# Kernel optimization log

Hardware: AMD Instinct MI355X
Metric: run time of the kernel (lower is better)

Reference implementation:

```python
import jax, jax.numpy as jnp
import numpy as np

MAX_ITER = 3


def setup_inputs() -> dict:
    key = jax.random.key(0)
    k1, k2, k3, k4 = jax.random.split(key, 4)
    B, S = 2, 160
    return {
        "s_edge": jax.random.normal(k1, (B, S, S), dtype=jnp.float32),
        "s_sib": jax.random.normal(k2, (B, S, S, S), dtype=jnp.float32),
        "s_cop": jax.random.normal(k3, (B, S, S, S), dtype=jnp.float32),
        "s_grd": jax.random.normal(k4, (B, S, S, S), dtype=jnp.float32),
        "mask": jnp.ones((B, S, S), dtype=bool),
    }


def _belief_propagation(s_edge, s_sib, s_cop, s_grd, mask):
    B, S, _ = mask.shape
    idx = jnp.arange(S)
    i, j = idx[:, None], idx[None, :]
    hs = jnp.minimum(i, j)  # [S,S] = min(index_i, index_j)
    ms = jnp.maximum(i, j)  # [S,S]

    mask_t = jnp.transpose(mask, (2, 1, 0))  # [S,S,B]
    # mask2o[x,y,z,b] = mask_t[x,z,b] & mask_t[x,y,b] & (hs[x,y]!=z) & (ms[x,y]!=z)
    mask2o = mask_t[:, None, :, :] & mask_t[:, :, None, :]
    mask2o = mask2o & (hs[:, :, None] != idx)[:, :, :, None]
    mask2o = mask2o & (ms[:, :, None] != idx)[:, :, :, None]
    mask2o_f = mask2o.astype(s_edge.dtype)  # [S,S,S,B]

    # p_edge[k,j,i,b] = (k==1) * s_edge[b,i,j]
    p_edge = jnp.transpose(jnp.stack([jnp.zeros_like(s_edge), s_edge]), (0, 3, 2, 1))  # [2,S,S,B]
    p_sib = jnp.transpose(s_sib, (2, 1, 3, 0))  # [S,S,S,B]
    p_cop = jnp.transpose(s_cop, (2, 1, 3, 0))
    p_grd = jnp.transpose(s_grd, (2, 1, 3, 0))

    b = jnp.zeros((2, S, S, B), dtype=s_edge.dtype)
    m_sib = jnp.zeros((2, S, S, S, B), dtype=s_edge.dtype)
    m_cop = jnp.zeros_like(m_sib)
    m_grd = jnp.zeros_like(m_sib)

    def update(b, m_prev, p):
        m = b[:, :, :, None, :] - m_prev  # [2,S,S,S,B]
        m0 = jnp.logaddexp(m[0], m[1])
        m1 = jnp.logaddexp(m[0], m[1] + p)
        mm = jnp.swapaxes(jnp.stack([m0, m1]), 2, 3)
        return jax.nn.log_softmax(mm, axis=0)

    for _ in range(MAX_ITER):
        b = jax.nn.log_softmax(b, axis=0)
        m_sib = update(b, m_sib, p_sib)
        m_cop = update(b, m_cop, p_cop)
        m_grd = update(b, m_grd, p_grd)
        b = p_edge + jnp.sum((m_sib + m_cop + m_grd) * mask2o_f, axis=3)

    # [B,S,S,2] log-marginals
    return jax.nn.log_softmax(jnp.transpose(b, (3, 2, 1, 0)), axis=-1)


def reference(s_edge, s_sib, s_cop, s_grd, mask):
    logQ = _belief_propagation(s_edge, s_sib, s_cop, s_grd, mask)
    return jnp.exp(logQ)  # marginals [B,S,S,2]
```

## Files before the change

kernel.cpp:

```cpp
#include <hip/hip_runtime.h>
#include <hip/hip_fp16.h>


#define S    160
#define S2   25600
#define S3   4096000
#define STR  162
#define C2E  1.4426950408889634f

__device__ __forceinline__ float fexp2(float x) { return __builtin_amdgcn_exp2f(x); }
__device__ __forceinline__ float flog2(float x) { return __builtin_amdgcn_logf(x); }
__device__ __forceinline__ float frcp(float x)  { return __builtin_amdgcn_rcpf(x); }
__device__ __forceinline__ float cdb(float x) {
    return fminf(fmaxf(x, -45.f), 45.f);
}
__device__ __forceinline__ float sp2t(float tp) { return flog2(1.f + tp); }
__device__ __forceinline__ float Ff(float x, float tp) {
    float tx = fexp2(x);
    return flog2(1.f + tx * tp) - flog2(1.f + tx);
}
__device__ __forceinline__ const float* selT(int t, const float* a,
                                             const float* b, const float* c) {
    return (t == 0) ? a : (t == 1) ? b : c;
}

__global__ __launch_bounds__(960)
void k_fused(const float* __restrict__ s_sib, const float* __restrict__ s_cop,
             const float* __restrict__ s_grd, const float* __restrict__ s_edge,
             float* __restrict__ outp)
{
    int slice = blockIdx.x;
    int a = slice % S, n = slice / S;
    int tid = threadIdx.x;
    int u4 = tid % 40, r = tid / 40;
    int us = tid % S,  vs = tid / S;

    __shared__ __half tp3[3 * S * STR];
    __shared__ float  scr[1280];
    __shared__ float  db1s[S], db2s[S], E1[S], E2[S];

    float4 acc = make_float4(0.f, 0.f, 0.f, 0.f);
    float edg = 0.f;
    if (tid < S) edg = s_edge[n * S2 + tid * S + a] * C2E;
    #pragma unroll
    for (int t = 0; t < 3; ++t) {
        const float* g = selT(t, s_sib, s_cop, s_grd)
                       + (long)n * S3 + (long)a * S + u4 * 4;
        float4 pv[7];
        #pragma unroll
        for (int i = 0; i < 6; ++i)
            pv[i] = *(const float4*)(g + (long)(r + 24 * i) * S2);
        if (r < 16) pv[6] = *(const float4*)(g + (long)(r + 144) * S2);
        float4 P = make_float4(1.f, 1.f, 1.f, 1.f);
        #pragma unroll
        for (int i = 0; i < 7; ++i) {
            if (i == 6 && r >= 16) break;
            int v = r + 24 * i;
            float t0 = fexp2(pv[i].x * C2E), t1 = fexp2(pv[i].y * C2E);
            float t2 = fexp2(pv[i].z * C2E), t3 = fexp2(pv[i].w * C2E);
            P.x = __builtin_fmaf(P.x, t0, P.x);
            P.y = __builtin_fmaf(P.y, t1, P.y);
            P.z = __builtin_fmaf(P.z, t2, P.z);
            P.w = __builtin_fmaf(P.w, t3, P.w);
            __half* b = &tp3[t * (S * STR) + v * STR + u4 * 4];
            *(__half2*)(b)     = __floats2half2_rn(t0, t1);
            *(__half2*)(b + 2) = __floats2half2_rn(t2, t3);
        }
        acc.x += flog2(P.x); acc.y += flog2(P.y);
        acc.z += flog2(P.z); acc.w += flog2(P.w);
    }
    float4* scr4 = (float4*)scr;
    if (r < 8) scr4[r * 40 + u4] = acc;
    __syncthreads();
    if (r >= 8 && r < 16) {
        float4 o = scr4[(r - 8) * 40 + u4];
        o.x += acc.x; o.y += acc.y; o.z += acc.z; o.w += acc.w;
        scr4[(r - 8) * 40 + u4] = o;
    }
    __syncthreads();
    if (r >= 16) {
        float4 o = scr4[(r - 16) * 40 + u4];
        o.x += acc.x; o.y += acc.y; o.z += acc.z; o.w += acc.w;
        scr4[(r - 16) * 40 + u4] = o;
    }
    __syncthreads();
    if (tid < S) {
        int u = tid, cu4 = u >> 2, cc = u & 3;
        float s = 0.f;
        #pragma unroll
        for (int g2 = 0; g2 < 8; ++g2) s += scr[(g2 * 40 + cu4) * 4 + cc];
        float rr = edg + s - 480.f;
        #pragma unroll
        for (int t = 0; t < 3; ++t) {
            const __half* sl = &tp3[t * (S * STR)];
            float tpa = __half2float(sl[a * STR + u]);
            rr -= (sp2t(tpa) - 1.f);
            if (u != a) {
                float tpu = __half2float(sl[u * STR + u]);
                rr -= (sp2t(tpu) - 1.f);
            }
        }
        db1s[u] = rr;
        E1[u] = fexp2(cdb(rr) + 1.f);
    }
    __syncthreads();

    float d2acc = 0.f;
    #pragma unroll
    for (int t = 0; t < 3; ++t) {
        const __half* sl = &tp3[t * (S * STR)];
        for (int kb = 0; kb < 6; ++kb) {
            float tA[4], tB[4], Ev[4];
            #pragma unroll
            for (int j = 0; j < 4; ++j) {
                int v = (kb * 4 + j) * 6 + vs;
                tA[j] = __half2float(sl[v * STR + us]);
                tB[j] = __half2float(sl[us * STR + v]);
                Ev[j] = E1[v];
            }
            #pragma unroll
            for (int j = 0; j < 4; ++j) {
                float B1 = 1.f + tB[j];
                float nm = __builtin_fmaf(Ev[j], tA[j], B1);
                float dn = B1 + Ev[j];
                d2acc += flog2(nm) - flog2(dn);
            }
        }
        #pragma unroll
        for (int k = 24; k < 27; ++k) {
            int v = k * 6 + vs;
            if (v < S) {
                float tA = __half2float(sl[v * STR + us]);
                float tB = __half2float(sl[us * STR + v]);
                float B1 = 1.f + tB;
                float nm = __builtin_fmaf(E1[v], tA, B1);
                float dn = B1 + E1[v];
                d2acc += flog2(nm) - flog2(dn);
            }
        }
    }
    scr[vs * S + us] = d2acc;
    __syncthreads();
    if (tid < S) {
        int u = tid;
        float sw = scr[u] + scr[S + u] + scr[2 * S + u] + scr[3 * S + u]
                 + scr[4 * S + u] + scr[5 * S + u];
        float db1a1 = cdb(db1s[a]) + 1.f;
        float db1u1 = cdb(db1s[u]) + 1.f;
        float sum = 0.f;
        #pragma unroll
        for (int t = 0; t < 3; ++t) {
            const __half* sl = &tp3[t * (S * STR)];
            float tpa  = __half2float(sl[a * STR + u]);
            float tpba = __half2float(sl[u * STR + a]);
            sum += Ff(db1a1 - sp2t(tpba), tpa);
            if (u != a) {
                float tpu = __half2float(sl[u * STR + u]);
                sum += Ff(db1u1 - sp2t(tpu), tpu);
            }
        }
        float d2v = edg - sum + sw;
        db2s[u] = d2v;
        E2[u] = fexp2(cdb(d2v));
    }
    __syncthreads();

    float d3acc = 0.f;
    float E1u = E1[us];
    #pragma unroll
    for (int t = 0; t < 3; ++t) {
        const __half* sl = &tp3[t * (S * STR)];
        for (int kb = 0; kb < 6; ++kb) {
            float tA[4], tB[4], Ev[4];
            #pragma unroll
            for (int j = 0; j < 4; ++j) {
                int v = (kb * 4 + j) * 6 + vs;
                tA[j] = __half2float(sl[v * STR + us]);
                tB[j] = __half2float(sl[us * STR + v]);
                Ev[j] = E2[v];
            }
            #pragma unroll
            for (int j = 0; j < 4; ++j) {
                float A1 = 1.f + tA[j];
                float q  = A1 + E1u;
                float rr = __builtin_fmaf(E1u, tB[j], A1);
                float p  = Ev[j] * q;
                float nm = __builtin_fmaf(p, tA[j], rr);
                float dn = rr + p;
                d3acc += flog2(nm) - flog2(dn);
            }
        }
        #pragma unroll
        for (int k = 24; k < 27; ++k) {
            int v = k * 6 + vs;
            if (v < S) {
                float tA = __half2float(sl[v * STR + us]);
                float tB = __half2float(sl[us * STR + v]);
                float A1 = 1.f + tA;
                float q  = A1 + E1u;
                float rr = __builtin_fmaf(E1u, tB, A1);
                float p  = E2[v] * q;
                float nm = __builtin_fmaf(p, tA, rr);
                float dn = rr + p;
                d3acc += flog2(nm) - flog2(dn);
            }
        }
    }
    scr[vs * S + us] = d3acc;
    __syncthreads();
    if (tid < S) {
        int u = tid;
        float sw = scr[u] + scr[S + u] + scr[2 * S + u] + scr[3 * S + u]
                 + scr[4 * S + u] + scr[5 * S + u];
        float db1u1 = cdb(db1s[u]) + 1.f;
        float db2a = cdb(db2s[a]);
        float db2u = cdb(db2s[u]);
        float sum = 0.f;
        #pragma unroll
        for (int t = 0; t < 3; ++t) {
            const __half* sl = &tp3[t * (S * STR)];
            float tpa  = __half2float(sl[a * STR + u]);
            float tpba = __half2float(sl[u * STR + a]);
            float d2vu = Ff(db1u1 - sp2t(tpa), tpba);
            sum += Ff(db2a - d2vu, tpa);
            if (u != a) {
                float tpu = __half2float(sl[u * STR + u]);
                float d2  = Ff(db1u1 - sp2t(tpu), tpu);
                sum += Ff(db2u - d2, tpu);
            }
        }
        float s = edg - sum + sw;
        float sc  = fminf(fmaxf(s, -60.f), 60.f);
        float tsg = fexp2(-sc);
        float rr  = __fdividef(1.f, 1.f + tsg);
        long ob = ((long)(n * S + u) * S + a) * 2;
        *(float2*)(outp + ob) = make_float2(tsg * rr, rr);
    }
}

extern "C" void kernel_launch(void* const* d_in, const int* in_sizes, int n_in,
                              void* d_out, int out_size, void* d_ws, size_t ws_size,
                              hipStream_t stream) {
    const float* s_edge = (const float*)d_in[0];
    const float* s_sib  = (const float*)d_in[1];
    const float* s_cop  = (const float*)d_in[2];
    const float* s_grd  = (const float*)d_in[3];
    float* outp = (float*)d_out;
    (void)d_ws; (void)ws_size;

    k_fused<<<320, 960, 0, stream>>>(s_sib, s_cop, s_grd, s_edge, outp);
}
```

Before: 155.5 us.

## Process both batch slices per block, prefetching second batch into registers

Each block now handles both batch elements for one column index a, halving the grid to 160 blocks. The second batch's score loads and exp2 work are issued up front and held as packed half values in registers, then written to shared memory after the first batch finishes. This overlaps the second load with the first batch's compute. The d2 inner loop also pairs log2 calls by multiplying two arguments before one log. The risks are lower occupancy on a 256-CU device, since only 160 blocks run, plus heavy register pressure from 21 uint2 per thread.

Result: no change. 156.9 us (+0.9%).

```diff
diff --git a/kernel.cpp b/kernel.cpp
--- a/kernel.cpp
+++ b/kernel.cpp
@@ -10,7 +10,6 @@
 
 __device__ __forceinline__ float fexp2(float x) { return __builtin_amdgcn_exp2f(x); }
 __device__ __forceinline__ float flog2(float x) { return __builtin_amdgcn_logf(x); }
-__device__ __forceinline__ float frcp(float x)  { return __builtin_amdgcn_rcpf(x); }
 __device__ __forceinline__ float cdb(float x) {
     return fminf(fmaxf(x, -45.f), 45.f);
 }
@@ -29,8 +28,7 @@
              const float* __restrict__ s_grd, const float* __restrict__ s_edge,
              float* __restrict__ outp)
 {
-    int slice = blockIdx.x;
-    int a = slice % S, n = slice / S;
+    int a = blockIdx.x;
     int tid = threadIdx.x;
     int u4 = tid % 40, r = tid / 40;
     int us = tid % S,  vs = tid / S;
@@ -39,13 +37,10 @@
     __shared__ float  scr[1280];
     __shared__ float  db1s[S], db2s[S], E1[S], E2[S];
 
-    float4 acc = make_float4(0.f, 0.f, 0.f, 0.f);
-    float edg = 0.f;
-    if (tid < S) edg = s_edge[n * S2 + tid * S + a] * C2E;
+    float4 acc0 = make_float4(0.f, 0.f, 0.f, 0.f);
     #pragma unroll
     for (int t = 0; t < 3; ++t) {
-        const float* g = selT(t, s_sib, s_cop, s_grd)
-                       + (long)n * S3 + (long)a * S + u4 * 4;
+        const float* g = selT(t, s_sib, s_cop, s_grd) + (long)a * S + u4 * 4;
         float4 pv[7];
         #pragma unroll
         for (int i = 0; i < 6; ++i)
@@ -66,175 +61,227 @@
             *(__half2*)(b)     = __floats2half2_rn(t0, t1);
             *(__half2*)(b + 2) = __floats2half2_rn(t2, t3);
         }
-        acc.x += flog2(P.x); acc.y += flog2(P.y);
-        acc.z += flog2(P.z); acc.w += flog2(P.w);
-    }
-    float4* scr4 = (float4*)scr;
-    if (r < 8) scr4[r * 40 + u4] = acc;
-    __syncthreads();
-    if (r >= 8 && r < 16) {
-        float4 o = scr4[(r - 8) * 40 + u4];
-        o.x += acc.x; o.y += acc.y; o.z += acc.z; o.w += acc.w;
-        scr4[(r - 8) * 40 + u4] = o;
-    }
-    __syncthreads();
-    if (r >= 16) {
-        float4 o = scr4[(r - 16) * 40 + u4];
-        o.x += acc.x; o.y += acc.y; o.z += acc.z; o.w += acc.w;
-        scr4[(r - 16) * 40 + u4] = o;
-    }
-    __syncthreads();
+        acc0.x += flog2(P.x); acc0.y += flog2(P.y);
+        acc0.z += flog2(P.z); acc0.w += flog2(P.w);
+    }
+    float4 acc1 = make_float4(0.f, 0.f, 0.f, 0.f);
+    uint2 ha1[21];
+    #pragma unroll
+    for (int t = 0; t < 3; ++t) {
+        const float* g = selT(t, s_sib, s_cop, s_grd) + S3 + (long)a * S + u4 * 4;
+        float4 pv[7];
+        #pragma unroll
+        for (int i = 0; i < 6; ++i)
+            pv[i] = *(const float4*)(g + (long)(r + 24 * i) * S2);
+        if (r < 16) pv[6] = *(const float4*)(g + (long)(r + 144) * S2);
+        float4 P = make_float4(1.f, 1.f, 1.f, 1.f);
+        #pragma unroll
+        for (int i = 0; i < 7; ++i) {
+            if (i == 6 && r >= 16) break;
+            float t0 = fexp2(pv[i].x * C2E), t1 = fexp2(pv[i].y * C2E);
+            float t2 = fexp2(pv[i].z * C2E), t3 = fexp2(pv[i].w * C2E);
+            P.x = __builtin_fmaf(P.x, t0, P.x);
+            P.y = __builtin_fmaf(P.y, t1, P.y);
+            P.z = __builtin_fmaf(P.z, t2, P.z);
+            P.w = __builtin_fmaf(P.w, t3, P.w);
+            __half2 h01 = __floats2half2_rn(t0, t1);
+            __half2 h23 = __floats2half2_rn(t2, t3);
+            ha1[t * 7 + i].x = *(unsigned*)&h01;
+            ha1[t * 7 + i].y = *(unsigned*)&h23;
+        }
+        acc1.x += flog2(P.x); acc1.y += flog2(P.y);
+        acc1.z += flog2(P.z); acc1.w += flog2(P.w);
+    }
+    float edg0 = 0.f, edg1 = 0.f;
     if (tid < S) {
-        int u = tid, cu4 = u >> 2, cc = u & 3;
-        float s = 0.f;
-        #pragma unroll
-        for (int g2 = 0; g2 < 8; ++g2) s += scr[(g2 * 40 + cu4) * 4 + cc];
-        float rr = edg + s - 480.f;
+        edg0 = s_edge[tid * S + a] * C2E;
+        edg1 = s_edge[S2 + tid * S + a] * C2E;
+    }
+
+    #pragma unroll 1
+    for (int ns = 0; ns < 2; ++ns) {
+        if (ns == 1) {
+            #pragma unroll
+            for (int t = 0; t < 3; ++t)
+                #pragma unroll
+                for (int i = 0; i < 7; ++i) {
+                    if (i == 6 && r >= 16) break;
+                    int v = r + 24 * i;
+                    *(uint2*)(&tp3[t * (S * STR) + v * STR + u4 * 4]) = ha1[t * 7 + i];
+                }
+            __syncthreads();
+        }
+        float4 accC = ns ? acc1 : acc0;
+        float  edgC = ns ? edg1 : edg0;
+        float4* scr4 = (float4*)scr;
+        if (r < 8) scr4[r * 40 + u4] = accC;
+        __syncthreads();
+        if (r >= 8 && r < 16) {
+            float4 o = scr4[(r - 8) * 40 + u4];
+            o.x += accC.x; o.y += accC.y; o.z += accC.z; o.w += accC.w;
+            scr4[(r - 8) * 40 + u4] = o;
+        }
+        __syncthreads();
+        if (r >= 16) {
+            float4 o = scr4[(r - 16) * 40 + u4];
+            o.x += accC.x; o.y += accC.y; o.z += accC.z; o.w += accC.w;
+            scr4[(r - 16) * 40 + u4] = o;
+        }
+        __syncthreads();
+        if (tid < S) {
+            int u = tid, cu4 = u >> 2, cc = u & 3;
+            float s = 0.f;
+            #pragma unroll
+            for (int g2 = 0; g2 < 8; ++g2) s += scr[(g2 * 40 + cu4) * 4 + cc];
+            float rr = edgC + s - 480.f;
+            #pragma unroll
+            for (int t = 0; t < 3; ++t) {
+                const __half* sl = &tp3[t * (S * STR)];
+                float tpa = __half2float(sl[a * STR + u]);
+                rr -= (sp2t(tpa) - 1.f);
+                if (u != a) {
+                    float tpu = __half2float(sl[u * STR + u]);
+                    rr -= (sp2t(tpu) - 1.f);
+                }
+            }
+            db1s[u] = rr;
+            E1[u] = fexp2(cdb(rr) + 1.f);
+        }
+        __syncthreads();
+
+        float d2acc = 0.f;
         #pragma unroll
         for (int t = 0; t < 3; ++t) {
             const __half* sl = &tp3[t * (S * STR)];
-            float tpa = __half2float(sl[a * STR + u]);
-            rr -= (sp2t(tpa) - 1.f);
-            if (u != a) {
-                float tpu = __half2float(sl[u * STR + u]);
-                rr -= (sp2t(tpu) - 1.f);
-            }
-        }
-        db1s[u] = rr;
-        E1[u] = fexp2(cdb(rr) + 1.f);
-    }
-    __syncthreads();
-
-    float d2acc = 0.f;
-    #pragma unroll
-    for (int t = 0; t < 3; ++t) {
-        const __half* sl = &tp3[t * (S * STR)];
-        for (int kb = 0; kb < 6; ++kb) {
-            float tA[4], tB[4], Ev[4];
-            #pragma unroll
-            for (int j = 0; j < 4; ++j) {
-                int v = (kb * 4 + j) * 6 + vs;
-                tA[j] = __half2float(sl[v * STR + us]);
-                tB[j] = __half2float(sl[us * STR + v]);
-                Ev[j] = E1[v];
-            }
-            #pragma unroll
-            for (int j = 0; j < 4; ++j) {
-                float B1 = 1.f + tB[j];
-                float nm = __builtin_fmaf(Ev[j], tA[j], B1);
-                float dn = B1 + Ev[j];
-                d2acc += flog2(nm) - flog2(dn);
-            }
-        }
-        #pragma unroll
-        for (int k = 24; k < 27; ++k) {
-            int v = k * 6 + vs;
-            if (v < S) {
-                float tA = __half2float(sl[v * STR + us]);
-                float tB = __half2float(sl[us * STR + v]);
-                float B1 = 1.f + tB;
-                float nm = __builtin_fmaf(E1[v], tA, B1);
-                float dn = B1 + E1[v];
-                d2acc += flog2(nm) - flog2(dn);
-            }
-        }
-    }
-    scr[vs * S + us] = d2acc;
-    __syncthreads();
-    if (tid < S) {
-        int u = tid;
-        float sw = scr[u] + scr[S + u] + scr[2 * S + u] + scr[3 * S + u]
-                 + scr[4 * S + u] + scr[5 * S + u];
-        float db1a1 = cdb(db1s[a]) + 1.f;
-        float db1u1 = cdb(db1s[u]) + 1.f;
-        float sum = 0.f;
+            for (int kb = 0; kb < 6; ++kb) {
+                float tA[4], tB[4], Ev[4], nm[4], dn[4];
+                #pragma unroll
+                for (int j = 0; j < 4; ++j) {
+                    int v = (kb * 4 + j) * 6 + vs;
+                    tA[j] = __half2float(sl[v * STR + us]);
+                    tB[j] = __half2float(sl[us * STR + v]);
+                    Ev[j] = E1[v];
+                }
+                #pragma unroll
+                for (int j = 0; j < 4; ++j) {
+                    float B1 = 1.f + tB[j];
+                    nm[j] = __builtin_fmaf(Ev[j], tA[j], B1);
+                    dn[j] = B1 + Ev[j];
+                }
+                d2acc += flog2(nm[0] * nm[1]) - flog2(dn[0] * dn[1]);
+                d2acc += flog2(nm[2] * nm[3]) - flog2(dn[2] * dn[3]);
+            }
+            #pragma unroll
+            for (int k = 24; k < 27; ++k) {
+                int v = k * 6 + vs;
+                if (v < S) {
+                    float tA = __half2float(sl[v * STR + us]);
+                    float tB = __half2float(sl[us * STR + v]);
+                    float B1 = 1.f + tB;
+                    float nm = __builtin_fmaf(E1[v], tA, B1);
+                    float dn = B1 + E1[v];
+                    d2acc += flog2(nm) - flog2(dn);
+                }
+            }
+        }
+        scr[vs * S + us] = d2acc;
+        __syncthreads();
+        if (tid < S) {
+            int u = tid;
+            float sw = scr[u] + scr[S + u] + scr[2 * S + u] + scr[3 * S + u]
+                     + scr[4 * S + u] + scr[5 * S + u];
+            float db1a1 = cdb(db1s[a]) + 1.f;
+            float db1u1 = cdb(db1s[u]) + 1.f;
+            float sum = 0.f;
+            #pragma unroll
+            for (int t = 0; t < 3; ++t) {
+                const __half* sl = &tp3[t * (S * STR)];
+                float tpa  = __half2float(sl[a * STR + u]);
+                float tpba = __half2float(sl[u * STR + a]);
+                sum += Ff(db1a1 - sp2t(tpba), tpa);
+                if (u != a) {
+                    float tpu = __half2float(sl[u * STR + u]);
+                    sum += Ff(db1u1 - sp2t(tpu), tpu);
+                }
+            }
+            float d2v = edgC - sum + sw;
+            db2s[u] = d2v;
+            E2[u] = fexp2(cdb(d2v));
+        }
+        __syncthreads();
+
+        float d3acc = 0.f;
+        float E1u = E1[us];
         #pragma unroll
         for (int t = 0; t < 3; ++t) {
             const __half* sl = &tp3[t * (S * STR)];
-            float tpa  = __half2float(sl[a * STR + u]);
-            float tpba = __half2float(sl[u * STR + a]);
-            sum += Ff(db1a1 - sp2t(tpba), tpa);
-            if (u != a) {
-                float tpu = __half2float(sl[u * STR + u]);
-                sum += Ff(db1u1 - sp2t(tpu), tpu);
-            }
-        }
-        float d2v = edg - sum + sw;
-        db2s[u] = d2v;
-        E2[u] = fexp2(cdb(d2v));
-    }
-    __syncthreads();
-
-    float d3acc = 0.f;
-    float E1u = E1[us];
-    #pragma unroll
-    for (int t = 0; t < 3; ++t) {
-        const __half* sl = &tp3[t * (S * STR)];
-        for (int kb = 0; kb < 6; ++kb) {
-            float tA[4], tB[4], Ev[4];
-            #pragma unroll
-            for (int j = 0; j < 4; ++j) {
-                int v = (kb * 4 + j) * 6 + vs;
-                tA[j] = __half2float(sl[v * STR + us]);
-                tB[j] = __half2float(sl[us * STR + v]);
-                Ev[j] = E2[v];
-            }
-            #pragma unroll
-            for (int j = 0; j < 4; ++j) {
-                float A1 = 1.f + tA[j];
-                float q  = A1 + E1u;
-                float rr = __builtin_fmaf(E1u, tB[j], A1);
-                float p  = Ev[j] * q;
-                float nm = __builtin_fmaf(p, tA[j], rr);
-                float dn = rr + p;
-                d3acc += flog2(nm) - flog2(dn);
-            }
-        }
-        #pragma unroll
-        for (int k = 24; k < 27; ++k) {
-            int v = k * 6 + vs;
-            if (v < S) {
-                float tA = __half2float(sl[v * STR + us]);
-                float tB = __half2float(sl[us * STR + v]);
-                float A1 = 1.f + tA;
-                float q  = A1 + E1u;
-                float rr = __builtin_fmaf(E1u, tB, A1);
-                float p  = E2[v] * q;
-                float nm = __builtin_fmaf(p, tA, rr);
-                float dn = rr + p;
-                d3acc += flog2(nm) - flog2(dn);
-            }
-        }
-    }
-    scr[vs * S + us] = d3acc;
-    __syncthreads();
-    if (tid < S) {
-        int u = tid;
-        float sw = scr[u] + scr[S + u] + scr[2 * S + u] + scr[3 * S + u]
-                 + scr[4 * S + u] + scr[5 * S + u];
-        float db1u1 = cdb(db1s[u]) + 1.f;
-        float db2a = cdb(db2s[a]);
-        float db2u = cdb(db2s[u]);
-        float sum = 0.f;
-        #pragma unroll
-        for (int t = 0; t < 3; ++t) {
-            const __half* sl = &tp3[t * (S * STR)];
-            float tpa  = __half2float(sl[a * STR + u]);
-            float tpba = __half2float(sl[u * STR + a]);
-            float d2vu = Ff(db1u1 - sp2t(tpa), tpba);
-            sum += Ff(db2a - d2vu, tpa);
-            if (u != a) {
-                float tpu = __half2float(sl[u * STR + u]);
-                float d2  = Ff(db1u1 - sp2t(tpu), tpu);
-                sum += Ff(db2u - d2, tpu);
-            }
-        }
-        float s = edg - sum + sw;
-        float sc  = fminf(fmaxf(s, -60.f), 60.f);
-        float tsg = fexp2(-sc);
-        float rr  = __fdividef(1.f, 1.f + tsg);
-        long ob = ((long)(n * S + u) * S + a) * 2;
-        *(float2*)(outp + ob) = make_float2(tsg * rr, rr);
+            for (int kb = 0; kb < 6; ++kb) {
+                float tA[4], tB[4], Ev[4];
+                #pragma unroll
+                for (int j = 0; j < 4; ++j) {
+                    int v = (kb * 4 + j) * 6 + vs;
+                    tA[j] = __half2float(sl[v * STR + us]);
+                    tB[j] = __half2float(sl[us * STR + v]);
+                    Ev[j] = E2[v];
+                }
+                #pragma unroll
+                for (int j = 0; j < 4; ++j) {
+                    float A1 = 1.f + tA[j];
+                    float q  = A1 + E1u;
+                    float rr = __builtin_fmaf(E1u, tB[j], A1);
+                    float p  = Ev[j] * q;
+                    float nm = __builtin_fmaf(p, tA[j], rr);
+                    float dn = rr + p;
+                    d3acc += flog2(nm) - flog2(dn);
+                }
+            }
+            #pragma unroll
+            for (int k = 24; k < 27; ++k) {
+                int v = k * 6 + vs;
+                if (v < S) {
+                    float tA = __half2float(sl[v * STR + us]);
+                    float tB = __half2float(sl[us * STR + v]);
+                    float A1 = 1.f + tA;
+                    float q  = A1 + E1u;
+                    float rr = __builtin_fmaf(E1u, tB, A1);
+                    float p  = E2[v] * q;
+                    float nm = __builtin_fmaf(p, tA, rr);
+                    float dn = rr + p;
+                    d3acc += flog2(nm) - flog2(dn);
+                }
+            }
+        }
+        scr[vs * S + us] = d3acc;
+        __syncthreads();
+        if (tid < S) {
+            int u = tid;
+            float sw = scr[u] + scr[S + u] + scr[2 * S + u] + scr[3 * S + u]
+                     + scr[4 * S + u] + scr[5 * S + u];
+            float db1u1 = cdb(db1s[u]) + 1.f;
+            float db2a = cdb(db2s[a]);
+            float db2u = cdb(db2s[u]);
+            float sum = 0.f;
+            #pragma unroll
+            for (int t = 0; t < 3; ++t) {
+                const __half* sl = &tp3[t * (S * STR)];
+                float tpa  = __half2float(sl[a * STR + u]);
+                float tpba = __half2float(sl[u * STR + a]);
+                float d2vu = Ff(db1u1 - sp2t(tpa), tpba);
+                sum += Ff(db2a - d2vu, tpa);
+                if (u != a) {
+                    float tpu = __half2float(sl[u * STR + u]);
+                    float d2  = Ff(db1u1 - sp2t(tpu), tpu);
+                    sum += Ff(db2u - d2, tpu);
+                }
+            }
+            float s = edgC - sum + sw;
+            float sc  = fminf(fmaxf(s, -60.f), 60.f);
+            float tsg = fexp2(-sc);
+            float rr  = __fdividef(1.f, 1.f + tsg);
+            long ob = ((long)(ns * S + u) * S + a) * 2;
+            *(float2*)(outp + ob) = make_float2(tsg * rr, rr);
+        }
+        if (ns == 0) __syncthreads();
     }
 }
 
@@ -248,5 +295,5 @@
     float* outp = (float*)d_out;
     (void)d_ws; (void)ws_size;
 
-    k_fused<<<320, 960, 0, stream>>>(s_sib, s_cop, s_grd, s_edge, outp);
-}
+    k_fused<<<160, 960, 0, stream>>>(s_sib, s_cop, s_grd, s_edge, outp);
+}
```

## Use single shared slab and re-stream score tensors per phase

Applied to the files above, without the earlier changes.

Replaces the three resident half-precision score slabs in shared memory with a single slab. Each of the three factor types is reloaded from global memory and re-exponentiated before its pass in phases 2 and 3. The row, column and diagonal entries needed by the per-u epilogues are kept in small side arrays. The block drops from 960 to 640 threads, and the phase-2 log pairs are merged by multiplying before taking the log. This cuts shared memory use (which could allow more blocks per CU) at the cost of extra global reads, extra exp work and extra barriers.

New measurement: 172.6 us. +11.0%, slower.

```diff
diff --git a/kernel.cpp b/kernel.cpp
--- a/kernel.cpp
+++ b/kernel.cpp
@@ -10,7 +10,6 @@
 
 __device__ __forceinline__ float fexp2(float x) { return __builtin_amdgcn_exp2f(x); }
 __device__ __forceinline__ float flog2(float x) { return __builtin_amdgcn_logf(x); }
-__device__ __forceinline__ float frcp(float x)  { return __builtin_amdgcn_rcpf(x); }
 __device__ __forceinline__ float cdb(float x) {
     return fminf(fmaxf(x, -45.f), 45.f);
 }
@@ -23,8 +22,11 @@
                                              const float* b, const float* c) {
     return (t == 0) ? a : (t == 1) ? b : c;
 }
-
-__global__ __launch_bounds__(960)
+__device__ __forceinline__ __half hsel(__half2 h01, __half2 h23, int c) {
+    return (c == 0) ? h01.x : (c == 1) ? h01.y : (c == 2) ? h23.x : h23.y;
+}
+
+__global__ __launch_bounds__(640)
 void k_fused(const float* __restrict__ s_sib, const float* __restrict__ s_cop,
              const float* __restrict__ s_grd, const float* __restrict__ s_edge,
              float* __restrict__ outp)
@@ -35,68 +37,82 @@
     int u4 = tid % 40, r = tid / 40;
     int us = tid % S,  vs = tid / S;
 
-    __shared__ __half tp3[3 * S * STR];
+    __shared__ __half slab[S * STR];
     __shared__ float  scr[1280];
     __shared__ float  db1s[S], db2s[S], E1[S], E2[S];
+    __shared__ __half rowA[3][S], colA[3][S], diagA[3][S];
+
+    const int aq = a >> 2, ac = a & 3;
 
     float4 acc = make_float4(0.f, 0.f, 0.f, 0.f);
-    float edg = 0.f;
-    if (tid < S) edg = s_edge[n * S2 + tid * S + a] * C2E;
     #pragma unroll
     for (int t = 0; t < 3; ++t) {
         const float* g = selT(t, s_sib, s_cop, s_grd)
                        + (long)n * S3 + (long)a * S + u4 * 4;
-        float4 pv[7];
-        #pragma unroll
-        for (int i = 0; i < 6; ++i)
-            pv[i] = *(const float4*)(g + (long)(r + 24 * i) * S2);
-        if (r < 16) pv[6] = *(const float4*)(g + (long)(r + 144) * S2);
+        float4 pv[10];
+        #pragma unroll
+        for (int i = 0; i < 10; ++i)
+            pv[i] = *(const float4*)(g + (long)(r + 16 * i) * S2);
         float4 P = make_float4(1.f, 1.f, 1.f, 1.f);
-        #pragma unroll
-        for (int i = 0; i < 7; ++i) {
-            if (i == 6 && r >= 16) break;
-            int v = r + 24 * i;
+        float4 Q = make_float4(1.f, 1.f, 1.f, 1.f);
+        #pragma unroll
+        for (int i = 0; i < 10; ++i) {
+            int v = r + 16 * i;
             float t0 = fexp2(pv[i].x * C2E), t1 = fexp2(pv[i].y * C2E);
             float t2 = fexp2(pv[i].z * C2E), t3 = fexp2(pv[i].w * C2E);
-            P.x = __builtin_fmaf(P.x, t0, P.x);
-            P.y = __builtin_fmaf(P.y, t1, P.y);
-            P.z = __builtin_fmaf(P.z, t2, P.z);
-            P.w = __builtin_fmaf(P.w, t3, P.w);
-            __half* b = &tp3[t * (S * STR) + v * STR + u4 * 4];
-            *(__half2*)(b)     = __floats2half2_rn(t0, t1);
-            *(__half2*)(b + 2) = __floats2half2_rn(t2, t3);
-        }
-        acc.x += flog2(P.x); acc.y += flog2(P.y);
-        acc.z += flog2(P.z); acc.w += flog2(P.w);
-    }
+            if (i < 5) {
+                P.x = __builtin_fmaf(P.x, t0, P.x);
+                P.y = __builtin_fmaf(P.y, t1, P.y);
+                P.z = __builtin_fmaf(P.z, t2, P.z);
+                P.w = __builtin_fmaf(P.w, t3, P.w);
+            } else {
+                Q.x = __builtin_fmaf(Q.x, t0, Q.x);
+                Q.y = __builtin_fmaf(Q.y, t1, Q.y);
+                Q.z = __builtin_fmaf(Q.z, t2, Q.z);
+                Q.w = __builtin_fmaf(Q.w, t3, Q.w);
+            }
+            __half2 h01 = __floats2half2_rn(t0, t1);
+            __half2 h23 = __floats2half2_rn(t2, t3);
+            if (t == 2) {
+                uint2 w; w.x = *(unsigned*)&h01; w.y = *(unsigned*)&h23;
+                *(uint2*)(&slab[v * STR + u4 * 4]) = w;
+            }
+            if (v == a) {
+                uint2 w; w.x = *(unsigned*)&h01; w.y = *(unsigned*)&h23;
+                *(uint2*)(&rowA[t][u4 * 4]) = w;
+            }
+            if (u4 == aq) colA[t][v] = hsel(h01, h23, ac);
+            if (u4 == (v >> 2)) diagA[t][v] = hsel(h01, h23, v & 3);
+        }
+        acc.x += flog2(P.x) + flog2(Q.x);
+        acc.y += flog2(P.y) + flog2(Q.y);
+        acc.z += flog2(P.z) + flog2(Q.z);
+        acc.w += flog2(P.w) + flog2(Q.w);
+    }
+    float edg = 0.f;
+    if (tid < S) edg = s_edge[(long)n * S2 + tid * S + a] * C2E;
+    __syncthreads();
     float4* scr4 = (float4*)scr;
     if (r < 8) scr4[r * 40 + u4] = acc;
     __syncthreads();
-    if (r >= 8 && r < 16) {
+    if (r >= 8) {
         float4 o = scr4[(r - 8) * 40 + u4];
         o.x += acc.x; o.y += acc.y; o.z += acc.z; o.w += acc.w;
         scr4[(r - 8) * 40 + u4] = o;
     }
     __syncthreads();
-    if (r >= 16) {
-        float4 o = scr4[(r - 16) * 40 + u4];
-        o.x += acc.x; o.y += acc.y; o.z += acc.z; o.w += acc.w;
-        scr4[(r - 16) * 40 + u4] = o;
-    }
-    __syncthreads();
     if (tid < S) {
-        int u = tid, cu4 = u >> 2, cc = u & 3;
+        int u = tid;
         float s = 0.f;
         #pragma unroll
-        for (int g2 = 0; g2 < 8; ++g2) s += scr[(g2 * 40 + cu4) * 4 + cc];
+        for (int g2 = 0; g2 < 8; ++g2) s += scr[(g2 * 40 + (u >> 2)) * 4 + (u & 3)];
         float rr = edg + s - 480.f;
         #pragma unroll
         for (int t = 0; t < 3; ++t) {
-            const __half* sl = &tp3[t * (S * STR)];
-            float tpa = __half2float(sl[a * STR + u]);
+            float tpa = __half2float(rowA[t][u]);
             rr -= (sp2t(tpa) - 1.f);
             if (u != a) {
-                float tpu = __half2float(sl[u * STR + u]);
+                float tpu = __half2float(diagA[t][u]);
                 rr -= (sp2t(tpu) - 1.f);
             }
         }
@@ -106,56 +122,62 @@
     __syncthreads();
 
     float d2acc = 0.f;
-    #pragma unroll
-    for (int t = 0; t < 3; ++t) {
-        const __half* sl = &tp3[t * (S * STR)];
-        for (int kb = 0; kb < 6; ++kb) {
-            float tA[4], tB[4], Ev[4];
-            #pragma unroll
-            for (int j = 0; j < 4; ++j) {
-                int v = (kb * 4 + j) * 6 + vs;
-                tA[j] = __half2float(sl[v * STR + us]);
-                tB[j] = __half2float(sl[us * STR + v]);
+    #pragma unroll 1
+    for (int tt = 0; tt < 3; ++tt) {
+        int t = (tt == 0) ? 2 : tt - 1;
+        if (tt != 0) {
+            __syncthreads();
+            const float* g = selT(t, s_sib, s_cop, s_grd)
+                           + (long)n * S3 + (long)a * S + u4 * 4;
+            float4 pv[10];
+            #pragma unroll
+            for (int i = 0; i < 10; ++i)
+                pv[i] = *(const float4*)(g + (long)(r + 16 * i) * S2);
+            #pragma unroll
+            for (int i = 0; i < 10; ++i) {
+                float t0 = fexp2(pv[i].x * C2E), t1 = fexp2(pv[i].y * C2E);
+                float t2 = fexp2(pv[i].z * C2E), t3 = fexp2(pv[i].w * C2E);
+                __half2 h01 = __floats2half2_rn(t0, t1);
+                __half2 h23 = __floats2half2_rn(t2, t3);
+                uint2 w; w.x = *(unsigned*)&h01; w.y = *(unsigned*)&h23;
+                *(uint2*)(&slab[(r + 16 * i) * STR + u4 * 4]) = w;
+            }
+            __syncthreads();
+        }
+        for (int kb = 0; kb < 10; ++kb) {
+            float tA[4], tB[4], Ev[4], nm[4], dn[4];
+            #pragma unroll
+            for (int j = 0; j < 4; ++j) {
+                int v = kb * 16 + j * 4 + vs;
+                tA[j] = __half2float(slab[v * STR + us]);
+                tB[j] = __half2float(slab[us * STR + v]);
                 Ev[j] = E1[v];
             }
             #pragma unroll
             for (int j = 0; j < 4; ++j) {
                 float B1 = 1.f + tB[j];
-                float nm = __builtin_fmaf(Ev[j], tA[j], B1);
-                float dn = B1 + Ev[j];
-                d2acc += flog2(nm) - flog2(dn);
-            }
-        }
-        #pragma unroll
-        for (int k = 24; k < 27; ++k) {
-            int v = k * 6 + vs;
-            if (v < S) {
-                float tA = __half2float(sl[v * STR + us]);
-                float tB = __half2float(sl[us * STR + v]);
-                float B1 = 1.f + tB;
-                float nm = __builtin_fmaf(E1[v], tA, B1);
-                float dn = B1 + E1[v];
-                d2acc += flog2(nm) - flog2(dn);
-            }
+                nm[j] = __builtin_fmaf(Ev[j], tA[j], B1);
+                dn[j] = B1 + Ev[j];
+            }
+            d2acc += flog2(nm[0] * nm[1]) - flog2(dn[0] * dn[1]);
+            d2acc += flog2(nm[2] * nm[3]) - flog2(dn[2] * dn[3]);
         }
     }
     scr[vs * S + us] = d2acc;
     __syncthreads();
     if (tid < S) {
         int u = tid;
-        float sw = scr[u] + scr[S + u] + scr[2 * S + u] + scr[3 * S + u]
-                 + scr[4 * S + u] + scr[5 * S + u];
+        float sw = scr[u] + scr[S + u] + scr[2 * S + u] + scr[3 * S + u];
         float db1a1 = cdb(db1s[a]) + 1.f;
         float db1u1 = cdb(db1s[u]) + 1.f;
         float sum = 0.f;
         #pragma unroll
         for (int t = 0; t < 3; ++t) {
-            const __half* sl = &tp3[t * (S * STR)];
-            float tpa  = __half2float(sl[a * STR + u]);
-            float tpba = __half2float(sl[u * STR + a]);
+            float tpa  = __half2float(rowA[t][u]);
+            float tpba = __half2float(colA[t][u]);
             sum += Ff(db1a1 - sp2t(tpba), tpa);
             if (u != a) {
-                float tpu = __half2float(sl[u * STR + u]);
+                float tpu = __half2float(diagA[t][u]);
                 sum += Ff(db1u1 - sp2t(tpu), tpu);
             }
         }
@@ -167,16 +189,35 @@
 
     float d3acc = 0.f;
     float E1u = E1[us];
-    #pragma unroll
-    for (int t = 0; t < 3; ++t) {
-        const __half* sl = &tp3[t * (S * STR)];
-        for (int kb = 0; kb < 6; ++kb) {
+    #pragma unroll 1
+    for (int tt = 0; tt < 3; ++tt) {
+        int t = (tt == 0) ? 1 : (tt == 1) ? 2 : 0;
+        if (tt != 0) {
+            __syncthreads();
+            const float* g = selT(t, s_sib, s_cop, s_grd)
+                           + (long)n * S3 + (long)a * S + u4 * 4;
+            float4 pv[10];
+            #pragma unroll
+            for (int i = 0; i < 10; ++i)
+                pv[i] = *(const float4*)(g + (long)(r + 16 * i) * S2);
+            #pragma unroll
+            for (int i = 0; i < 10; ++i) {
+                float t0 = fexp2(pv[i].x * C2E), t1 = fexp2(pv[i].y * C2E);
+                float t2 = fexp2(pv[i].z * C2E), t3 = fexp2(pv[i].w * C2E);
+                __half2 h01 = __floats2half2_rn(t0, t1);
+                __half2 h23 = __floats2half2_rn(t2, t3);
+                uint2 w; w.x = *(unsigned*)&h01; w.y = *(unsigned*)&h23;
+                *(uint2*)(&slab[(r + 16 * i) * STR + u4 * 4]) = w;
+            }
+            __syncthreads();
+        }
+        for (int kb = 0; kb < 10; ++kb) {
             float tA[4], tB[4], Ev[4];
             #pragma unroll
             for (int j = 0; j < 4; ++j) {
-                int v = (kb * 4 + j) * 6 + vs;
-                tA[j] = __half2float(sl[v * STR + us]);
-                tB[j] = __half2float(sl[us * STR + v]);
+                int v = kb * 16 + j * 4 + vs;
+                tA[j] = __half2float(slab[v * STR + us]);
+                tB[j] = __half2float(slab[us * STR + v]);
                 Ev[j] = E2[v];
             }
             #pragma unroll
@@ -190,41 +231,24 @@
                 d3acc += flog2(nm) - flog2(dn);
             }
         }
-        #pragma unroll
-        for (int k = 24; k < 27; ++k) {
-            int v = k * 6 + vs;
-            if (v < S) {
-                float tA = __half2float(sl[v * STR + us]);
-                float tB = __half2float(sl[us * STR + v]);
-                float A1 = 1.f + tA;
-                float q  = A1 + E1u;
-                float rr = __builtin_fmaf(E1u, tB, A1);
-                float p  = E2[v] * q;
-                float nm = __builtin_fmaf(p, tA, rr);
-                float dn = rr + p;
-                d3acc += flog2(nm) - flog2(dn);
-            }
-        }
     }
     scr[vs * S + us] = d3acc;
     __syncthreads();
     if (tid < S) {
         int u = tid;
-        float sw = scr[u] + scr[S + u] + scr[2 * S + u] + scr[3 * S + u]
-                 + scr[4 * S + u] + scr[5 * S + u];
+        float sw = scr[u] + scr[S + u] + scr[2 * S + u] + scr[3 * S + u];
         float db1u1 = cdb(db1s[u]) + 1.f;
         float db2a = cdb(db2s[a]);
         float db2u = cdb(db2s[u]);
         float sum = 0.f;
         #pragma unroll
         for (int t = 0; t < 3; ++t) {
-            const __half* sl = &tp3[t * (S * STR)];
-            float tpa  = __half2float(sl[a * STR + u]);
-            float tpba = __half2float(sl[u * STR + a]);
+            float tpa  = __half2float(rowA[t][u]);
+            float tpba = __half2float(colA[t][u]);
             float d2vu = Ff(db1u1 - sp2t(tpa), tpba);
             sum += Ff(db2a - d2vu, tpa);
             if (u != a) {
-                float tpu = __half2float(sl[u * STR + u]);
+                float tpu = __half2float(diagA[t][u]);
                 float d2  = Ff(db1u1 - sp2t(tpu), tpu);
                 sum += Ff(db2u - d2, tpu);
             }
@@ -248,5 +272,5 @@
     float* outp = (float*)d_out;
     (void)d_ws; (void)ws_size;
 
-    k_fused<<<320, 960, 0, stream>>>(s_sib, s_cop, s_grd, s_edge, outp);
-}
+    k_fused<<<320, 640, 0, stream>>>(s_sib, s_cop, s_grd, s_edge, outp);
+}
```

## Register-tile the pairwise passes into 4x8 blocks with vectorized half loads

Applied to the files above, without the earlier changes.

Rewrites the two O(S^2) inner passes so each thread handles a 4(u) x 8(v) tile. Both the tA rows and the transposed tB values are fetched with 64-bit shared loads, and E values with float4 loads. It also pairs the logarithms by multiplying two arguments before one log2, which halves the transcendental count in the d2 pass. The goal is to cut LDS instruction count and log2 throughput cost. In exchange only 800 of 960 threads do work, the reduction takes an extra barrier stage, the row stride grows to 164 for alignment, and the paired-product log adds some overflow or precision risk.

Result: slower. 185.4 us (+19.2%).

```diff
diff --git a/kernel.cpp b/kernel.cpp
--- a/kernel.cpp
+++ b/kernel.cpp
@@ -5,12 +5,11 @@
 #define S    160
 #define S2   25600
 #define S3   4096000
-#define STR  162
+#define STR  164
 #define C2E  1.4426950408889634f
 
 __device__ __forceinline__ float fexp2(float x) { return __builtin_amdgcn_exp2f(x); }
 __device__ __forceinline__ float flog2(float x) { return __builtin_amdgcn_logf(x); }
-__device__ __forceinline__ float frcp(float x)  { return __builtin_amdgcn_rcpf(x); }
 __device__ __forceinline__ float cdb(float x) {
     return fminf(fmaxf(x, -45.f), 45.f);
 }
@@ -23,6 +22,14 @@
                                              const float* b, const float* c) {
     return (t == 0) ? a : (t == 1) ? b : c;
 }
+__device__ __forceinline__ float hlo(unsigned u) {
+    __half2 h = *(__half2*)&u; return __low2float(h);
+}
+__device__ __forceinline__ float hhi(unsigned u) {
+    __half2 h = *(__half2*)&u; return __high2float(h);
+}
+#define HEXT(av, i) ((i)==0 ? hlo((av).x) : (i)==1 ? hhi((av).x) : \
+                     (i)==2 ? hlo((av).y) : hhi((av).y))
 
 __global__ __launch_bounds__(960)
 void k_fused(const float* __restrict__ s_sib, const float* __restrict__ s_cop,
@@ -33,15 +40,17 @@
     int a = slice % S, n = slice / S;
     int tid = threadIdx.x;
     int u4 = tid % 40, r = tid / 40;
-    int us = tid % S,  vs = tid / S;
-
-    __shared__ __half tp3[3 * S * STR];
-    __shared__ float  scr[1280];
-    __shared__ float  db1s[S], db2s[S], E1[S], E2[S];
+
+    __shared__ __align__(16) __half tp3[3 * S * STR];
+    __shared__ __align__(16) float  scr[800];
+    __shared__ __align__(16) float  db1s[S];
+    __shared__ __align__(16) float  db2s[S];
+    __shared__ __align__(16) float  E1[S];
+    __shared__ __align__(16) float  E2[S];
 
     float4 acc = make_float4(0.f, 0.f, 0.f, 0.f);
     float edg = 0.f;
-    if (tid < S) edg = s_edge[n * S2 + tid * S + a] * C2E;
+    if (tid < S) edg = s_edge[(long)n * S2 + tid * S + a] * C2E;
     #pragma unroll
     for (int t = 0; t < 3; ++t) {
         const float* g = selT(t, s_sib, s_cop, s_grd)
@@ -70,25 +79,37 @@
         acc.z += flog2(P.z); acc.w += flog2(P.w);
     }
     float4* scr4 = (float4*)scr;
-    if (r < 8) scr4[r * 40 + u4] = acc;
-    __syncthreads();
-    if (r >= 8 && r < 16) {
-        float4 o = scr4[(r - 8) * 40 + u4];
+    if (r < 5) scr4[r * 40 + u4] = acc;
+    __syncthreads();
+    if (r >= 5 && r < 10) {
+        float4 o = scr4[(r - 5) * 40 + u4];
         o.x += acc.x; o.y += acc.y; o.z += acc.z; o.w += acc.w;
-        scr4[(r - 8) * 40 + u4] = o;
-    }
-    __syncthreads();
-    if (r >= 16) {
-        float4 o = scr4[(r - 16) * 40 + u4];
+        scr4[(r - 5) * 40 + u4] = o;
+    }
+    __syncthreads();
+    if (r >= 10 && r < 15) {
+        float4 o = scr4[(r - 10) * 40 + u4];
         o.x += acc.x; o.y += acc.y; o.z += acc.z; o.w += acc.w;
-        scr4[(r - 16) * 40 + u4] = o;
+        scr4[(r - 10) * 40 + u4] = o;
+    }
+    __syncthreads();
+    if (r >= 15 && r < 20) {
+        float4 o = scr4[(r - 15) * 40 + u4];
+        o.x += acc.x; o.y += acc.y; o.z += acc.z; o.w += acc.w;
+        scr4[(r - 15) * 40 + u4] = o;
+    }
+    __syncthreads();
+    if (r >= 20) {
+        float4 o = scr4[(r - 20) * 40 + u4];
+        o.x += acc.x; o.y += acc.y; o.z += acc.z; o.w += acc.w;
+        scr4[(r - 20) * 40 + u4] = o;
     }
     __syncthreads();
     if (tid < S) {
-        int u = tid, cu4 = u >> 2, cc = u & 3;
+        int u = tid;
         float s = 0.f;
         #pragma unroll
-        for (int g2 = 0; g2 < 8; ++g2) s += scr[(g2 * 40 + cu4) * 4 + cc];
+        for (int g2 = 0; g2 < 5; ++g2) s += scr[(g2 * 40 + (u >> 2)) * 4 + (u & 3)];
         float rr = edg + s - 480.f;
         #pragma unroll
         for (int t = 0; t < 3; ++t) {
@@ -105,46 +126,74 @@
     }
     __syncthreads();
 
-    float d2acc = 0.f;
-    #pragma unroll
-    for (int t = 0; t < 3; ++t) {
-        const __half* sl = &tp3[t * (S * STR)];
-        for (int kb = 0; kb < 6; ++kb) {
-            float tA[4], tB[4], Ev[4];
-            #pragma unroll
-            for (int j = 0; j < 4; ++j) {
-                int v = (kb * 4 + j) * 6 + vs;
-                tA[j] = __half2float(sl[v * STR + us]);
-                tB[j] = __half2float(sl[us * STR + v]);
-                Ev[j] = E1[v];
-            }
-            #pragma unroll
-            for (int j = 0; j < 4; ++j) {
-                float B1 = 1.f + tB[j];
-                float nm = __builtin_fmaf(Ev[j], tA[j], B1);
-                float dn = B1 + Ev[j];
-                d2acc += flog2(nm) - flog2(dn);
-            }
-        }
-        #pragma unroll
-        for (int k = 24; k < 27; ++k) {
-            int v = k * 6 + vs;
-            if (v < S) {
-                float tA = __half2float(sl[v * STR + us]);
-                float tB = __half2float(sl[us * STR + v]);
-                float B1 = 1.f + tB;
-                float nm = __builtin_fmaf(E1[v], tA, B1);
-                float dn = B1 + E1[v];
-                d2acc += flog2(nm) - flog2(dn);
-            }
-        }
-    }
-    scr[vs * S + us] = d2acc;
+    const bool act = (r < 20);
+    const int u0 = u4 * 4, v0 = r * 8;
+    float4 ac2 = make_float4(0.f, 0.f, 0.f, 0.f);
+    if (act) {
+        #pragma unroll
+        for (int t = 0; t < 3; ++t) {
+            const __half* sl = &tp3[t * (S * STR)];
+            uint2 avr[8];
+            #pragma unroll
+            for (int j = 0; j < 8; ++j)
+                avr[j] = *(const uint2*)&sl[(v0 + j) * STR + u0];
+            uint2 b0[4], b1[4];
+            #pragma unroll
+            for (int i = 0; i < 4; ++i) {
+                b0[i] = *(const uint2*)&sl[(u0 + i) * STR + v0];
+                b1[i] = *(const uint2*)&sl[(u0 + i) * STR + v0 + 4];
+            }
+            float Ev[8];
+            *(float4*)&Ev[0] = *(const float4*)&E1[v0];
+            *(float4*)&Ev[4] = *(const float4*)&E1[v0 + 4];
+            #pragma unroll
+            for (int i = 0; i < 4; ++i) {
+                float tB[8];
+                tB[0] = hlo(b0[i].x); tB[1] = hhi(b0[i].x);
+                tB[2] = hlo(b0[i].y); tB[3] = hhi(b0[i].y);
+                tB[4] = hlo(b1[i].x); tB[5] = hhi(b1[i].x);
+                tB[6] = hlo(b1[i].y); tB[7] = hhi(b1[i].y);
+                float s = 0.f;
+                #pragma unroll
+                for (int jp = 0; jp < 4; ++jp) {
+                    float tA0 = HEXT(avr[2 * jp], i);
+                    float tA1 = HEXT(avr[2 * jp + 1], i);
+                    float B10 = 1.f + tB[2 * jp], B11 = 1.f + tB[2 * jp + 1];
+                    float nm0 = __builtin_fmaf(Ev[2 * jp], tA0, B10);
+                    float nm1 = __builtin_fmaf(Ev[2 * jp + 1], tA1, B11);
+                    float dn0 = B10 + Ev[2 * jp], dn1 = B11 + Ev[2 * jp + 1];
+                    s += flog2(nm0 * nm1) - flog2(dn0 * dn1);
+                }
+                if (i == 0) ac2.x += s; else if (i == 1) ac2.y += s;
+                else if (i == 2) ac2.z += s; else ac2.w += s;
+            }
+        }
+    }
+    if (act && r < 5) scr4[r * 40 + u4] = ac2;
+    __syncthreads();
+    if (act && r >= 5 && r < 10) {
+        float4 o = scr4[(r - 5) * 40 + u4];
+        o.x += ac2.x; o.y += ac2.y; o.z += ac2.z; o.w += ac2.w;
+        scr4[(r - 5) * 40 + u4] = o;
+    }
+    __syncthreads();
+    if (act && r >= 10 && r < 15) {
+        float4 o = scr4[(r - 10) * 40 + u4];
+        o.x += ac2.x; o.y += ac2.y; o.z += ac2.z; o.w += ac2.w;
+        scr4[(r - 10) * 40 + u4] = o;
+    }
+    __syncthreads();
+    if (act && r >= 15) {
+        float4 o = scr4[(r - 15) * 40 + u4];
+        o.x += ac2.x; o.y += ac2.y; o.z += ac2.z; o.w += ac2.w;
+        scr4[(r - 15) * 40 + u4] = o;
+    }
     __syncthreads();
     if (tid < S) {
         int u = tid;
-        float sw = scr[u] + scr[S + u] + scr[2 * S + u] + scr[3 * S + u]
-                 + scr[4 * S + u] + scr[5 * S + u];
+        float sw = 0.f;
+        #pragma unroll
+        for (int g2 = 0; g2 < 5; ++g2) sw += scr[(g2 * 40 + (u >> 2)) * 4 + (u & 3)];
         float db1a1 = cdb(db1s[a]) + 1.f;
         float db1u1 = cdb(db1s[u]) + 1.f;
         float sum = 0.f;
@@ -165,53 +214,76 @@
     }
     __syncthreads();
 
-    float d3acc = 0.f;
-    float E1u = E1[us];
-    #pragma unroll
-    for (int t = 0; t < 3; ++t) {
-        const __half* sl = &tp3[t * (S * STR)];
-        for (int kb = 0; kb < 6; ++kb) {
-            float tA[4], tB[4], Ev[4];
-            #pragma unroll
-            for (int j = 0; j < 4; ++j) {
-                int v = (kb * 4 + j) * 6 + vs;
-                tA[j] = __half2float(sl[v * STR + us]);
-                tB[j] = __half2float(sl[us * STR + v]);
-                Ev[j] = E2[v];
-            }
-            #pragma unroll
-            for (int j = 0; j < 4; ++j) {
-                float A1 = 1.f + tA[j];
-                float q  = A1 + E1u;
-                float rr = __builtin_fmaf(E1u, tB[j], A1);
-                float p  = Ev[j] * q;
-                float nm = __builtin_fmaf(p, tA[j], rr);
-                float dn = rr + p;
-                d3acc += flog2(nm) - flog2(dn);
-            }
-        }
-        #pragma unroll
-        for (int k = 24; k < 27; ++k) {
-            int v = k * 6 + vs;
-            if (v < S) {
-                float tA = __half2float(sl[v * STR + us]);
-                float tB = __half2float(sl[us * STR + v]);
-                float A1 = 1.f + tA;
-                float q  = A1 + E1u;
-                float rr = __builtin_fmaf(E1u, tB, A1);
-                float p  = E2[v] * q;
-                float nm = __builtin_fmaf(p, tA, rr);
-                float dn = rr + p;
-                d3acc += flog2(nm) - flog2(dn);
-            }
-        }
-    }
-    scr[vs * S + us] = d3acc;
+    float4 ac3 = make_float4(0.f, 0.f, 0.f, 0.f);
+    float E1u[4];
+    *(float4*)E1u = *(const float4*)&E1[u0];
+    if (act) {
+        #pragma unroll
+        for (int t = 0; t < 3; ++t) {
+            const __half* sl = &tp3[t * (S * STR)];
+            uint2 avr[8];
+            #pragma unroll
+            for (int j = 0; j < 8; ++j)
+                avr[j] = *(const uint2*)&sl[(v0 + j) * STR + u0];
+            uint2 b0[4], b1[4];
+            #pragma unroll
+            for (int i = 0; i < 4; ++i) {
+                b0[i] = *(const uint2*)&sl[(u0 + i) * STR + v0];
+                b1[i] = *(const uint2*)&sl[(u0 + i) * STR + v0 + 4];
+            }
+            float Ev[8];
+            *(float4*)&Ev[0] = *(const float4*)&E2[v0];
+            *(float4*)&Ev[4] = *(const float4*)&E2[v0 + 4];
+            #pragma unroll
+            for (int i = 0; i < 4; ++i) {
+                float tB[8];
+                tB[0] = hlo(b0[i].x); tB[1] = hhi(b0[i].x);
+                tB[2] = hlo(b0[i].y); tB[3] = hhi(b0[i].y);
+                tB[4] = hlo(b1[i].x); tB[5] = hhi(b1[i].x);
+                tB[6] = hlo(b1[i].y); tB[7] = hhi(b1[i].y);
+                float e1i = E1u[i];
+                float s = 0.f;
+                #pragma unroll
+                for (int j = 0; j < 8; ++j) {
+                    float tA = HEXT(avr[j], i);
+                    float A1 = 1.f + tA;
+                    float q  = A1 + e1i;
+                    float rr = __builtin_fmaf(e1i, tB[j], A1);
+                    float p  = Ev[j] * q;
+                    float nm = __builtin_fmaf(p, tA, rr);
+                    float dn = rr + p;
+                    s += flog2(nm) - flog2(dn);
+                }
+                if (i == 0) ac3.x += s; else if (i == 1) ac3.y += s;
+                else if (i == 2) ac3.z += s; else ac3.w += s;
+            }
+        }
+    }
+    if (act && r < 5) scr4[r * 40 + u4] = ac3;
+    __syncthreads();
+    if (act && r >= 5 && r < 10) {
+        float4 o = scr4[(r - 5) * 40 + u4];
+        o.x += ac3.x; o.y += ac3.y; o.z += ac3.z; o.w += ac3.w;
+        scr4[(r - 5) * 40 + u4] = o;
+    }
+    __syncthreads();
+    if (act && r >= 10 && r < 15) {
+        float4 o = scr4[(r - 10) * 40 + u4];
+        o.x += ac3.x; o.y += ac3.y; o.z += ac3.z; o.w += ac3.w;
+        scr4[(r - 10) * 40 + u4] = o;
+    }
+    __syncthreads();
+    if (act && r >= 15) {
+        float4 o = scr4[(r - 15) * 40 + u4];
+        o.x += ac3.x; o.y += ac3.y; o.z += ac3.z; o.w += ac3.w;
+        scr4[(r - 15) * 40 + u4] = o;
+    }
     __syncthreads();
     if (tid < S) {
         int u = tid;
-        float sw = scr[u] + scr[S + u] + scr[2 * S + u] + scr[3 * S + u]
-                 + scr[4 * S + u] + scr[5 * S + u];
+        float sw = 0.f;
+        #pragma unroll
+        for (int g2 = 0; g2 < 5; ++g2) sw += scr[(g2 * 40 + (u >> 2)) * 4 + (u & 3)];
         float db1u1 = cdb(db1s[u]) + 1.f;
         float db2a = cdb(db2s[a]);
         float db2u = cdb(db2s[u]);
```
